# Kernel tuning notes

Measured on AMD Instinct MI355X. Metric: run time of the kernel, lower is better.

The kernel has to match this reference:

```python
import jax, jax.numpy as jnp
import numpy as np

# --- static config (lmax = mmax = 2, m-prime coefficient layout) ---
L = 2
NCOEF = (L + 1) ** 2            # 9 coeffs; m-prime order: m=0 -> l=0,1,2 | m=1 -> (-,+) x l=1,2 | m=2 -> (-,+) x l=2
GATE_IDX = jnp.array([0, 1, 0, 1, 0, 1, 1, 1])  # (l-1) of each non-scalar coeff in m-prime order
N_NODES = 10000
N_EDGES = 50000
C_SPH = 128
C_HID = 128
C_EDGE = 128
EXTRA_M0 = L * C_HID            # gate scalars emitted by conv1's m=0 branch


def _silu(x):
    return x * jax.nn.sigmoid(x)


def _layernorm(x, g, b, eps=1e-5):
    mu = jnp.mean(x, axis=-1, keepdims=True)
    var = jnp.var(x, axis=-1, keepdims=True)
    return (x - mu) * jax.lax.rsqrt(var + eps) * g + b


def _radial(x_edge, w1, b1, g, beta, w2, b2):
    # RadialFunction: Linear -> LayerNorm -> SiLU -> Linear, emits per-edge channel weights [E, 6*c_in]
    h = _silu(_layernorm(x_edge @ w1 + b1, g, beta))
    return h @ w2 + b2


def _so2_conv(feat, rad, w0, b0, w1, w2, c_in, c_out, extra):
    # feat: [E, 9, c_in] in m-prime order. Block-diagonal SO2 conv with per-edge radial modulation.
    E = feat.shape[0]
    # m = 0 block (3 real coeffs) -> dense linear, optionally emits extra gating scalars
    x0 = feat[:, 0:3].reshape(E, 3 * c_in) * rad[:, : 3 * c_in]
    y0 = x0 @ w0 + b0                                   # [E, 3*c_out + extra]
    out0 = y0[:, : 3 * c_out].reshape(E, 3, c_out)
    x_extra = y0[:, 3 * c_out:]
    # m = 1 block: coeffs 3:7 -> [E, 2(sign), 2(l)*c_in], complex-structured matmul
    x1 = feat[:, 3:7].reshape(E, 2, 2 * c_in) * rad[:, 3 * c_in: 5 * c_in][:, None, :]
    y1 = x1 @ w1                                        # [E, 2, 4*c_out]
    h = 2 * c_out
    r, i = y1[..., :h], y1[..., h:]
    out1 = jnp.stack([r[:, 0] - i[:, 1], r[:, 1] + i[:, 0]], axis=1).reshape(E, 4, c_out)
    # m = 2 block: coeffs 7:9 -> [E, 2(sign), 1(l)*c_in]
    x2 = feat[:, 7:9].reshape(E, 2, c_in) * rad[:, 5 * c_in: 6 * c_in][:, None, :]
    y2 = x2 @ w2                                        # [E, 2, 2*c_out]
    r, i = y2[..., :c_out], y2[..., c_out:]
    out2 = jnp.stack([r[:, 0] - i[:, 1], r[:, 1] + i[:, 0]], axis=1).reshape(E, 2, c_out)
    return jnp.concatenate([out0, out1, out2], axis=1), x_extra


def _gate(gating, feat):
    # GateActivation (m_prime=True): SiLU on l=0 scalar, SiLU(gates) broadcast per-degree on l>0 coeffs
    E = feat.shape[0]
    g = _silu(gating).reshape(E, L, C_HID)[:, GATE_IDX]  # [E, 8, C_HID]
    return jnp.concatenate([_silu(feat[:, :1]), feat[:, 1:] * g], axis=1)


def setup_inputs() -> dict:
    key = jax.random.key(0)
    ks = jax.random.split(key, 16)

    def nrm(k, shape, scale=1.0):
        return jax.random.normal(k, shape, dtype=jnp.float32) * scale

    C, H, CE = C_SPH, C_HID, C_EDGE
    return {
        "x": nrm(ks[0], (N_NODES, NCOEF, C)),
        "x_edge": nrm(ks[1], (N_EDGES, CE)),
        "edge_distance": jax.random.uniform(ks[2], (N_EDGES,), dtype=jnp.float32),
        "edge_index": jax.random.randint(ks[3], (2, N_EDGES), 0, N_NODES),
        "wigner": nrm(ks[4], (N_EDGES, NCOEF, NCOEF), 0.3),
        "wigner_inv": nrm(ks[5], (N_EDGES, NCOEF, NCOEF), 0.3),
        # radial MLP 1 (edge embed -> 6*C_SPH per-edge weights)
        "rad1_w1": nrm(ks[6], (CE, CE), CE ** -0.5),
        "rad1_b1": jnp.zeros((CE,), jnp.float32),
        "rad1_g": jnp.ones((CE,), jnp.float32),
        "rad1_beta": jnp.zeros((CE,), jnp.float32),
        "rad1_w2": nrm(ks[7], (CE, 6 * C), CE ** -0.5),
        "rad1_b2": jnp.zeros((6 * C,), jnp.float32),
        # SO2 conv 1 (sphere -> hidden, + gate scalars)
        "c1_w0": nrm(ks[8], (3 * C, 3 * H + EXTRA_M0), (3 * C) ** -0.5),
        "c1_b0": jnp.zeros((3 * H + EXTRA_M0,), jnp.float32),
        "c1_w1": nrm(ks[9], (2 * C, 4 * H), (2 * C) ** -0.5),
        "c1_w2": nrm(ks[10], (C, 2 * H), C ** -0.5),
        # radial MLP 2 (edge embed -> 6*C_HID per-edge weights)
        "rad2_w1": nrm(ks[11], (CE, CE), CE ** -0.5),
        "rad2_b1": jnp.zeros((CE,), jnp.float32),
        "rad2_g": jnp.ones((CE,), jnp.float32),
        "rad2_beta": jnp.zeros((CE,), jnp.float32),
        "rad2_w2": nrm(ks[12], (CE, 6 * H), CE ** -0.5),
        "rad2_b2": jnp.zeros((6 * H,), jnp.float32),
        # SO2 conv 2 (hidden -> sphere)
        "c2_w0": nrm(ks[13], (3 * H, 3 * C), (3 * H) ** -0.5),
        "c2_b0": jnp.zeros((3 * C,), jnp.float32),
        "c2_w1": nrm(ks[14], (2 * H, 4 * C), (2 * H) ** -0.5),
        "c2_w2": nrm(ks[15], (H, 2 * C), H ** -0.5),
    }


def reference(x, x_edge, edge_distance, edge_index, wigner, wigner_inv,
              rad1_w1, rad1_b1, rad1_g, rad1_beta, rad1_w2, rad1_b2,
              c1_w0, c1_b0, c1_w1, c1_w2,
              rad2_w1, rad2_b1, rad2_g, rad2_beta, rad2_w2, rad2_b2,
              c2_w0, c2_b0, c2_w1, c2_w2):
    src, dst = edge_index[0], edge_index[1]
    # gather source node features + per-edge Wigner rotation into m-prime layout: [E, 9, C_SPH]
    msg = jnp.einsum('erf,efc->erc', wigner, x[src])
    rad1 = _radial(x_edge, rad1_w1, rad1_b1, rad1_g, rad1_beta, rad1_w2, rad1_b2)
    msg, gating = _so2_conv(msg, rad1, c1_w0, c1_b0, c1_w1, c1_w2, C_SPH, C_HID, EXTRA_M0)
    msg = _gate(gating, msg)
    rad2 = _radial(x_edge, rad2_w1, rad2_b1, rad2_g, rad2_beta, rad2_w2, rad2_b2)
    msg, _ = _so2_conv(msg, rad2, c2_w0, c2_b0, c2_w1, c2_w2, C_HID, C_SPH, 0)
    # rotate back to the global frame and scatter-sum onto destination nodes
    msg = jnp.einsum('efr,erc->efc', wigner_inv, msg)
    return jax.ops.segment_sum(msg, dst, num_segments=x.shape[0])
```

## Files before the change

kernel.cpp:

```cpp
#include <hip/hip_runtime.h>
#include <hip/hip_bf16.h>

#define EDGES 50000
#define NODES 10000

typedef __hip_bfloat16 bf16;
typedef __attribute__((ext_vector_type(8))) short bf16x8v;
typedef __attribute__((ext_vector_type(4))) float f32x4;

__device__ __forceinline__ float bf2f(bf16 v){ return __bfloat162float(v); }
__device__ __forceinline__ bf16  f2bf(float v){ return __float2bfloat16(v); }
__device__ __forceinline__ unsigned short f2bfu(float f){
  bf16 h = __float2bfloat16(f);
  union{ bf16 h; unsigned short s; } u; u.h = h; return u.s;
}
__device__ __forceinline__ float silu_f(float v){ return v * (1.0f/(1.0f+__expf(-v))); }

__device__ __forceinline__ unsigned mul1(unsigned a, unsigned b){
  union{unsigned u; float f;} a0,a1,b0,b1;
  a0.u = (a & 0xffffu) << 16; a1.u = a & 0xffff0000u;
  b0.u = (b & 0xffffu) << 16; b1.u = b & 0xffff0000u;
  float p0 = a0.f*b0.f, p1 = a1.f*b1.f;
  return (unsigned)f2bfu(p0) | ((unsigned)f2bfu(p1) << 16);
}
__device__ __forceinline__ uint4 mulp(uint4 a, uint4 b){
  uint4 r; r.x=mul1(a.x,b.x); r.y=mul1(a.y,b.y); r.z=mul1(a.z,b.z); r.w=mul1(a.w,b.w); return r;
}

__global__ __launch_bounds__(256)
void k_wT(const float* __restrict__ w, bf16* __restrict__ wt, int K, int N){
  __shared__ float tile[32][33];
  const int kb = blockIdx.x*32, nb = blockIdx.y*32;
  const int tx = threadIdx.x & 31, ty = threadIdx.x >> 5;
#pragma unroll
  for (int i=0;i<32;i+=8) tile[ty+i][tx] = w[(size_t)(kb+ty+i)*N + nb+tx];
  __syncthreads();
#pragma unroll
  for (int i=0;i<32;i+=8) wt[(size_t)(nb+ty+i)*K + kb+tx] = f2bf(tile[tx][ty+i]);
}

__global__ __launch_bounds__(128)
void k_gather_rot(const float* __restrict__ x, const int* __restrict__ eidx,
                  const float* __restrict__ wig, bf16* __restrict__ msg)
{
  const int e = blockIdx.x;
  const int c = threadIdx.x;
  __shared__ float wl[81];
  if (c < 81) wl[c] = wig[e*81 + c];
  const int src = eidx[e];
  const float* xp = x + (size_t)src*1152 + c;
  float xr[9];
#pragma unroll
  for (int f=0; f<9; ++f) xr[f] = xp[f*128];
  __syncthreads();
  bf16* mp = msg + (size_t)e*1152 + c;
#pragma unroll
  for (int fo=0; fo<9; ++fo){
    float a = 0.f;
#pragma unroll
    for (int f=0; f<9; ++f) a = fmaf(wl[fo*9+f], xr[f], a);
    mp[fo*128] = f2bf(a);
  }
}

__global__ __launch_bounds__(256)
void k_radial(const float* __restrict__ x_edge,
              const float* __restrict__ w1, const float* __restrict__ b1,
              const float* __restrict__ gm, const float* __restrict__ bt,
              const float* __restrict__ w2, const float* __restrict__ b2,
              bf16* __restrict__ ro)
{
  __shared__ float xe[16][128];
  __shared__ float h[16][128];
  __shared__ float mu_s[16], rs_s[16];
  const int t = threadIdx.x;
  const int e0 = blockIdx.x * 16;
  for (int i=0;i<8;++i){
    int lin = t + 256*i;
    int e = lin >> 7, j2 = lin & 127;
    xe[e][j2] = x_edge[(size_t)(e0+e)*128 + j2];
  }
  __syncthreads();
  const int j = t & 127, g = t >> 7;
  {
    float acc[8] = {0,0,0,0,0,0,0,0};
    for (int k=0;k<128;k+=4){
      float wv0 = w1[(k+0)*128+j];
      float wv1 = w1[(k+1)*128+j];
      float wv2 = w1[(k+2)*128+j];
      float wv3 = w1[(k+3)*128+j];
#pragma unroll
      for (int e=0;e<8;++e){
        float4 xv = *(const float4*)&xe[g*8+e][k];
        acc[e] += xv.x*wv0 + xv.y*wv1 + xv.z*wv2 + xv.w*wv3;
      }
    }
    float bv = b1[j];
#pragma unroll
    for (int e=0;e<8;++e) h[g*8+e][j] = acc[e] + bv;
  }
  __syncthreads();
  {
    int e = t >> 4, p = t & 15;
    float s=0.f, ss=0.f;
#pragma unroll
    for (int i=0;i<8;++i){ float v = h[e][p+16*i]; s += v; ss += v*v; }
#pragma unroll
    for (int off=8; off>0; off>>=1){ s += __shfl_xor(s, off, 16); ss += __shfl_xor(ss, off, 16); }
    if (p==0){
      float m = s*(1.f/128.f);
      mu_s[e] = m;
      rs_s[e] = rsqrtf(fmaxf(ss*(1.f/128.f)-m*m, 0.f) + 1e-5f);
    }
  }
  __syncthreads();
  {
    float gv = gm[j], bv = bt[j];
#pragma unroll
    for (int e=0;e<8;++e){
      int ee = g*8+e;
      float v = (h[ee][j]-mu_s[ee])*rs_s[ee]*gv + bv;
      h[ee][j] = silu_f(v);
    }
  }
  __syncthreads();
  if (t < 192){
    int col = t*4;
    float acc[16][4];
#pragma unroll
    for (int e=0;e<16;++e){ acc[e][0]=acc[e][1]=acc[e][2]=acc[e][3]=0.f; }
    for (int k=0;k<128;k+=4){
      float4 wv0 = *(const float4*)&w2[(k+0)*768+col];
      float4 wv1 = *(const float4*)&w2[(k+1)*768+col];
      float4 wv2 = *(const float4*)&w2[(k+2)*768+col];
      float4 wv3 = *(const float4*)&w2[(k+3)*768+col];
#pragma unroll
      for (int e=0;e<16;++e){
        float4 hv = *(const float4*)&h[e][k];
        acc[e][0] += hv.x*wv0.x + hv.y*wv1.x + hv.z*wv2.x + hv.w*wv3.x;
        acc[e][1] += hv.x*wv0.y + hv.y*wv1.y + hv.z*wv2.y + hv.w*wv3.y;
        acc[e][2] += hv.x*wv0.z + hv.y*wv1.z + hv.z*wv2.z + hv.w*wv3.z;
        acc[e][3] += hv.x*wv0.w + hv.y*wv1.w + hv.z*wv2.w + hv.w*wv3.w;
      }
    }
    float4 bv = *(const float4*)&b2[col];
#pragma unroll
    for (int e=0;e<16;++e){
      ushort4 pk;
      pk.x = f2bfu(acc[e][0]+bv.x);
      pk.y = f2bfu(acc[e][1]+bv.y);
      pk.z = f2bfu(acc[e][2]+bv.z);
      pk.w = f2bfu(acc[e][3]+bv.w);
      *reinterpret_cast<ushort4*>(&ro[(size_t)(e0+e)*768 + col]) = pk;
    }
  }
}

template<bool CONV1>
__global__ __launch_bounds__(256, 3)
void k_so2_mfma(const bf16* __restrict__ rad,
                const bf16* __restrict__ w0t, const float* __restrict__ b0,
                const bf16* __restrict__ w1t, const bf16* __restrict__ w2t,
                bf16* __restrict__ msg)
{
  __shared__ char ldsA[32768];
  __shared__ bf16 gls[8192];
  const int t    = threadIdx.x;
  const int lane = t & 63, wv = t >> 6;
  const int lrow = lane & 15, lhi = lane >> 4;
  const int e0 = blockIdx.x * 32;
  int evalid = EDGES - e0; if (evalid > 32) evalid = 32;

#pragma unroll
  for (int i=0;i<6;++i){
    int ch = t + 256*i;
    int row = ch / 48, k0 = (ch % 48) * 8;
    int e = e0 + row;
    uint4 o = {0u,0u,0u,0u};
    if (e < EDGES){
      uint4 mz = *(const uint4*)(msg + (size_t)e*1152 + k0);
      uint4 rz = *(const uint4*)(rad + (size_t)e*768  + k0);
      o = mulp(mz, rz);
    }
    *(uint4*)(ldsA + ((row*768 + k0*2) ^ ((row&7)<<4))) = o;
  }
  __syncthreads();

  constexpr int NT0 = CONV1 ? 10 : 6;
  const int wcol0 = wv * NT0 * 16;
  f32x4 acc0[NT0][2];
  const f32x4 zf = {0.f,0.f,0.f,0.f};
#pragma unroll
  for (int nt=0; nt<NT0; ++nt){ acc0[nt][0]=zf; acc0[nt][1]=zf; }
  for (int ks=0; ks<12; ++ks){
    bf16x8v a0 = *(const bf16x8v*)(ldsA + (((lrow   )*768 + ks*64 + lhi*16) ^ ((lrow&7)<<4)));
    bf16x8v a1 = *(const bf16x8v*)(ldsA + (((16+lrow)*768 + ks*64 + lhi*16) ^ ((lrow&7)<<4)));
#pragma unroll
    for (int nt=0; nt<NT0; ++nt){
      int coln = wcol0 + nt*16 + lrow;
      bf16x8v b = *(const bf16x8v*)(w0t + (size_t)coln*384 + ks*32 + lhi*8);
      acc0[nt][0] = __builtin_amdgcn_mfma_f32_16x16x32_bf16(a0, b, acc0[nt][0], 0,0,0);
      acc0[nt][1] = __builtin_amdgcn_mfma_f32_16x16x32_bf16(a1, b, acc0[nt][1], 0,0,0);
    }
  }
  if (CONV1){
#pragma unroll
    for (int nt=0; nt<NT0; ++nt){
      int colb = wcol0 + nt*16;
      if (colb >= 384){
        float bc = b0[colb + lrow];
#pragma unroll
        for (int mt=0; mt<2; ++mt)
#pragma unroll
        for (int r=0; r<4; ++r){
          int el = mt*16 + lhi*4 + r;
          gls[el*256 + colb + lrow - 384] = f2bf(silu_f(acc0[nt][mt][r] + bc));
        }
      }
    }
  }
  __syncthreads();
#pragma unroll
  for (int nt=0; nt<NT0; ++nt){
    int colb = wcol0 + nt*16;
    if (colb < 384){
      int col = colb + lrow;
      int f = col >> 7, c = col & 127;
      float bc = b0[col];
#pragma unroll
      for (int mt=0; mt<2; ++mt)
#pragma unroll
      for (int r=0; r<4; ++r){
        int el = mt*16 + lhi*4 + r;
        if (el < evalid){
          float v = acc0[nt][mt][r] + bc;
          float o;
          if (CONV1) o = (f==0) ? silu_f(v) : v * bf2f(gls[el*256 + (f==2?128:0) + c]);
          else       o = v;
          msg[(size_t)(e0+el)*1152 + col] = f2bf(o);
        }
      }
    }
  }

#pragma unroll
  for (int i=0;i<8;++i){
    int ch = t + 256*i;
    int row = ch >> 5, k0 = (ch & 31) * 8;
    int e = e0 + (row >> 1);
    uint4 o = {0u,0u,0u,0u};
    if (e < EDGES){
      uint4 mz = *(const uint4*)(msg + (size_t)e*1152 + 384 + (row&1)*256 + k0);
      uint4 rz = *(const uint4*)(rad + (size_t)e*768  + 384 + k0);
      o = mulp(mz, rz);
    }
    *(uint4*)(ldsA + ((row*512 + k0*2) ^ ((row&7)<<4))) = o;
  }
  __syncthreads();

#pragma unroll
  for (int half=0; half<2; ++half){
    f32x4 acc1[4][2][2];
#pragma unroll
    for (int p=0;p<4;++p){ acc1[p][0][0]=zf; acc1[p][0][1]=zf; acc1[p][1][0]=zf; acc1[p][1][1]=zf; }
    for (int ks=0; ks<8; ++ks){
      bf16x8v aA[2];
#pragma unroll
      for (int m2=0; m2<2; ++m2){
        int row = (half*2+m2)*16 + lrow;
        aA[m2] = *(const bf16x8v*)(ldsA + ((row*512 + ks*64 + lhi*16) ^ ((row&7)<<4)));
      }
#pragma unroll
      for (int p=0; p<4; ++p){
        int jj = wv*64 + p*16 + lrow;
        bf16x8v br = *(const bf16x8v*)(w1t + (size_t)jj*256       + ks*32 + lhi*8);
        bf16x8v bi = *(const bf16x8v*)(w1t + (size_t)(jj+256)*256 + ks*32 + lhi*8);
#pragma unroll
        for (int m2=0;m2<2;++m2){
          acc1[p][m2][0] = __builtin_amdgcn_mfma_f32_16x16x32_bf16(aA[m2], br, acc1[p][m2][0], 0,0,0);
          acc1[p][m2][1] = __builtin_amdgcn_mfma_f32_16x16x32_bf16(aA[m2], bi, acc1[p][m2][1], 0,0,0);
        }
      }
    }
#pragma unroll
    for (int p=0;p<4;++p)
#pragma unroll
    for (int m2=0;m2<2;++m2){
      int mt = half*2 + m2;
#pragma unroll
      for (int re=0;re<2;++re){
        int el = mt*8 + lhi*2 + re;
        float r0 = acc1[p][m2][0][2*re+0], r1 = acc1[p][m2][0][2*re+1];
        float i0 = acc1[p][m2][1][2*re+0], i1 = acc1[p][m2][1][2*re+1];
        float o0 = r0 - i1, o1 = r1 + i0;
        int jj = wv*64 + p*16 + lrow;
        if (CONV1){ float g = bf2f(gls[el*256 + jj]); o0 *= g; o1 *= g; }
        if (el < evalid){
          size_t base = (size_t)(e0+el)*1152;
          msg[base + 384 + jj] = f2bf(o0);
          msg[base + 640 + jj] = f2bf(o1);
        }
      }
    }
  }
  __syncthreads();

#pragma unroll
  for (int i=0;i<4;++i){
    int ch = t + 256*i;
    int row = ch >> 4, k0 = (ch & 15) * 8;
    int e = e0 + (row >> 1);
    uint4 o = {0u,0u,0u,0u};
    if (e < EDGES){
      uint4 mz = *(const uint4*)(msg + (size_t)e*1152 + 896 + (row&1)*128 + k0);
      uint4 rz = *(const uint4*)(rad + (size_t)e*768  + 640 + k0);
      o = mulp(mz, rz);
    }
    *(uint4*)(ldsA + ((row*256 + k0*2) ^ ((row&7)<<4))) = o;
  }
  __syncthreads();

  {
    f32x4 acc2[2][4][2];
#pragma unroll
    for (int p=0;p<2;++p)
#pragma unroll
    for (int mt=0;mt<4;++mt){ acc2[p][mt][0]=zf; acc2[p][mt][1]=zf; }
    for (int ks=0; ks<4; ++ks){
      bf16x8v aA[4];
#pragma unroll
      for (int mt=0;mt<4;++mt){
        int row = mt*16 + lrow;
        aA[mt] = *(const bf16x8v*)(ldsA + ((row*256 + ks*64 + lhi*16) ^ ((row&7)<<4)));
      }
#pragma unroll
      for (int p=0;p<2;++p){
        int jj = wv*32 + p*16 + lrow;
        bf16x8v br = *(const bf16x8v*)(w2t + (size_t)jj*128       + ks*32 + lhi*8);
        bf16x8v bi = *(const bf16x8v*)(w2t + (size_t)(jj+128)*128 + ks*32 + lhi*8);
#pragma unroll
        for (int mt=0;mt<4;++mt){
          acc2[p][mt][0] = __builtin_amdgcn_mfma_f32_16x16x32_bf16(aA[mt], br, acc2[p][mt][0], 0,0,0);
          acc2[p][mt][1] = __builtin_amdgcn_mfma_f32_16x16x32_bf16(aA[mt], bi, acc2[p][mt][1], 0,0,0);
        }
      }
    }
#pragma unroll
    for (int p=0;p<2;++p)
#pragma unroll
    for (int mt=0;mt<4;++mt)
#pragma unroll
    for (int re=0;re<2;++re){
      int el = mt*8 + lhi*2 + re;
      float r0 = acc2[p][mt][0][2*re+0], r1 = acc2[p][mt][0][2*re+1];
      float i0 = acc2[p][mt][1][2*re+0], i1 = acc2[p][mt][1][2*re+1];
      float o0 = r0 - i1, o1 = r1 + i0;
      int jj = wv*32 + p*16 + lrow;
      if (CONV1){ float g = bf2f(gls[el*256 + 128 + jj]); o0 *= g; o1 *= g; }
      if (el < evalid){
        size_t base = (size_t)(e0+el)*1152;
        msg[base + 896  + jj] = f2bf(o0);
        msg[base + 1024 + jj] = f2bf(o1);
      }
    }
  }
}

__global__ __launch_bounds__(128)
void k_wiginv_scatter(const bf16* __restrict__ msg, const int* __restrict__ eidx,
                      const float* __restrict__ wiginv, float* __restrict__ out)
{
  const int e = blockIdx.x;
  const int c = threadIdx.x;
  __shared__ float wl[81];
  if (c < 81) wl[c] = wiginv[e*81 + c];
  float m[9];
#pragma unroll
  for (int r=0;r<9;++r) m[r] = bf2f(msg[(size_t)e*1152 + r*128 + c]);
  const int dst = eidx[EDGES + e];
  __syncthreads();
  float* op = out + (size_t)dst*1152 + c;
#pragma unroll
  for (int f=0;f<9;++f){
    float a = 0.f;
#pragma unroll
    for (int r=0;r<9;++r) a = fmaf(wl[f*9+r], m[r], a);
    atomicAdd(op + f*128, a);
  }
}

extern "C" void kernel_launch(void* const* d_in, const int* in_sizes, int n_in,
                              void* d_out, int out_size, void* d_ws, size_t ws_size,
                              hipStream_t stream)
{
  const float* x       = (const float*)d_in[0];
  const float* x_edge  = (const float*)d_in[1];
  const int*   eidx    = (const int*)  d_in[3];
  const float* wig     = (const float*)d_in[4];
  const float* wiginv  = (const float*)d_in[5];
  const float* r1w1    = (const float*)d_in[6];
  const float* r1b1    = (const float*)d_in[7];
  const float* r1g     = (const float*)d_in[8];
  const float* r1bt    = (const float*)d_in[9];
  const float* r1w2    = (const float*)d_in[10];
  const float* r1b2    = (const float*)d_in[11];
  const float* c1w0    = (const float*)d_in[12];
  const float* c1b0    = (const float*)d_in[13];
  const float* c1w1    = (const float*)d_in[14];
  const float* c1w2    = (const float*)d_in[15];
  const float* r2w1    = (const float*)d_in[16];
  const float* r2b1    = (const float*)d_in[17];
  const float* r2g     = (const float*)d_in[18];
  const float* r2bt    = (const float*)d_in[19];
  const float* r2w2    = (const float*)d_in[20];
  const float* r2b2    = (const float*)d_in[21];
  const float* c2w0    = (const float*)d_in[22];
  const float* c2b0    = (const float*)d_in[23];
  const float* c2w1    = (const float*)d_in[24];
  const float* c2w2    = (const float*)d_in[25];
  float* out = (float*)d_out;

  char* ws = (char*)d_ws;
  bf16* msg  = (bf16*)(ws);
  bf16* rad  = (bf16*)(ws + (size_t)115200000);
  bf16* w0t1 = (bf16*)(ws + (size_t)192000000);
  bf16* w1t1 = (bf16*)(ws + (size_t)192491520);
  bf16* w2t1 = (bf16*)(ws + (size_t)192753664);
  bf16* w0t2 = (bf16*)(ws + (size_t)192819200);
  bf16* w1t2 = (bf16*)(ws + (size_t)193114112);
  bf16* w2t2 = (bf16*)(ws + (size_t)193376256);

  k_wT<<<dim3(12,20),256,0,stream>>>(c1w0, w0t1, 384, 640);
  k_wT<<<dim3( 8,16),256,0,stream>>>(c1w1, w1t1, 256, 512);
  k_wT<<<dim3( 4, 8),256,0,stream>>>(c1w2, w2t1, 128, 256);
  k_wT<<<dim3(12,12),256,0,stream>>>(c2w0, w0t2, 384, 384);
  k_wT<<<dim3( 8,16),256,0,stream>>>(c2w1, w1t2, 256, 512);
  k_wT<<<dim3( 4, 8),256,0,stream>>>(c2w2, w2t2, 128, 256);

  hipMemsetAsync(d_out, 0, (size_t)out_size*sizeof(float), stream);
  k_gather_rot<<<EDGES, 128, 0, stream>>>(x, eidx, wig, msg);
  k_radial<<<EDGES/16, 256, 0, stream>>>(x_edge, r1w1, r1b1, r1g, r1bt, r1w2, r1b2, rad);
  k_so2_mfma<true ><<<(EDGES+31)/32, 256, 0, stream>>>(rad, w0t1, c1b0, w1t1, w2t1, msg);
  k_radial<<<EDGES/16, 256, 0, stream>>>(x_edge, r2w1, r2b1, r2g, r2bt, r2w2, r2b2, rad);
  k_so2_mfma<false><<<(EDGES+31)/32, 256, 0, stream>>>(rad, w0t2, c2b0, w1t2, w2t2, msg);
  k_wiginv_scatter<<<EDGES, 128, 0, stream>>>(msg, eidx, wiginv, out);
}
```

Baseline: 1.471 ms.

## Split fused SO2 conv kernel into per-m-block kernels with global gate buffer

The single fused SO2 conv kernel is split into three kernels, one per m-block (m=0, m=1, m=2), with the gate scalars written to a global buffer instead of shared memory. The m=1 kernel uses 16-edge blocks to create more blocks, and weight loads are batched ahead of the MFMA sequences to hide latency. The aim is smaller LDS per kernel, better occupancy and shorter dependency chains, at the cost of extra launches and re-reading msg, rad and gate data from global memory.

```diff
diff --git a/kernel.cpp b/kernel.cpp
--- a/kernel.cpp
+++ b/kernel.cpp
@@ -156,51 +156,60 @@
   }
 }
 
+
 template<bool CONV1>
 __global__ __launch_bounds__(256, 3)
-void k_so2_mfma(const bf16* __restrict__ rad,
-                const bf16* __restrict__ w0t, const float* __restrict__ b0,
-                const bf16* __restrict__ w1t, const bf16* __restrict__ w2t,
-                bf16* __restrict__ msg)
-{
-  __shared__ char ldsA[32768];
+void k_g0(const bf16* __restrict__ rad, const bf16* __restrict__ msg_in,
+          const bf16* __restrict__ w0t, const float* __restrict__ b0,
+          bf16* __restrict__ msg, bf16* __restrict__ glb)
+{
+  __shared__ char ldsA[24576];
   __shared__ bf16 gls[8192];
-  const int t    = threadIdx.x;
+  const int t = threadIdx.x;
   const int lane = t & 63, wv = t >> 6;
   const int lrow = lane & 15, lhi = lane >> 4;
   const int e0 = blockIdx.x * 32;
   int evalid = EDGES - e0; if (evalid > 32) evalid = 32;
+  const uint4 z4 = {0u,0u,0u,0u};
+  const f32x4 zf = {0.f,0.f,0.f,0.f};
 
 #pragma unroll
   for (int i=0;i<6;++i){
     int ch = t + 256*i;
     int row = ch / 48, k0 = (ch % 48) * 8;
     int e = e0 + row;
-    uint4 o = {0u,0u,0u,0u};
+    uint4 mz = z4, rz = z4;
     if (e < EDGES){
-      uint4 mz = *(const uint4*)(msg + (size_t)e*1152 + k0);
-      uint4 rz = *(const uint4*)(rad + (size_t)e*768  + k0);
-      o = mulp(mz, rz);
-    }
-    *(uint4*)(ldsA + ((row*768 + k0*2) ^ ((row&7)<<4))) = o;
+      mz = *(const uint4*)(msg_in + (size_t)e*1152 + k0);
+      rz = *(const uint4*)(rad    + (size_t)e*768  + k0);
+    }
+    *(uint4*)(ldsA + ((row*768 + k0*2) ^ ((row&7)<<4))) = mulp(mz, rz);
   }
   __syncthreads();
 
   constexpr int NT0 = CONV1 ? 10 : 6;
+  constexpr int HB  = NT0 / 2;
   const int wcol0 = wv * NT0 * 16;
   f32x4 acc0[NT0][2];
-  const f32x4 zf = {0.f,0.f,0.f,0.f};
 #pragma unroll
   for (int nt=0; nt<NT0; ++nt){ acc0[nt][0]=zf; acc0[nt][1]=zf; }
   for (int ks=0; ks<12; ++ks){
     bf16x8v a0 = *(const bf16x8v*)(ldsA + (((lrow   )*768 + ks*64 + lhi*16) ^ ((lrow&7)<<4)));
     bf16x8v a1 = *(const bf16x8v*)(ldsA + (((16+lrow)*768 + ks*64 + lhi*16) ^ ((lrow&7)<<4)));
 #pragma unroll
-    for (int nt=0; nt<NT0; ++nt){
-      int coln = wcol0 + nt*16 + lrow;
-      bf16x8v b = *(const bf16x8v*)(w0t + (size_t)coln*384 + ks*32 + lhi*8);
-      acc0[nt][0] = __builtin_amdgcn_mfma_f32_16x16x32_bf16(a0, b, acc0[nt][0], 0,0,0);
-      acc0[nt][1] = __builtin_amdgcn_mfma_f32_16x16x32_bf16(a1, b, acc0[nt][1], 0,0,0);
+    for (int h=0; h<2; ++h){
+      bf16x8v bb[HB];
+#pragma unroll
+      for (int j=0;j<HB;++j){
+        int coln = wcol0 + (h*HB+j)*16 + lrow;
+        bb[j] = *(const bf16x8v*)(w0t + (size_t)coln*384 + ks*32 + lhi*8);
+      }
+#pragma unroll
+      for (int j=0;j<HB;++j){
+        int nt = h*HB+j;
+        acc0[nt][0] = __builtin_amdgcn_mfma_f32_16x16x32_bf16(a0, bb[j], acc0[nt][0], 0,0,0);
+        acc0[nt][1] = __builtin_amdgcn_mfma_f32_16x16x32_bf16(a1, bb[j], acc0[nt][1], 0,0,0);
+      }
     }
   }
   if (CONV1){
@@ -209,17 +218,20 @@
       int colb = wcol0 + nt*16;
       if (colb >= 384){
         float bc = b0[colb + lrow];
+        int cc = colb + lrow - 384;
 #pragma unroll
         for (int mt=0; mt<2; ++mt)
 #pragma unroll
         for (int r=0; r<4; ++r){
           int el = mt*16 + lhi*4 + r;
-          gls[el*256 + colb + lrow - 384] = f2bf(silu_f(acc0[nt][mt][r] + bc));
+          bf16 gv = f2bf(silu_f(acc0[nt][mt][r] + bc));
+          gls[el*256 + cc] = gv;
+          if (el < evalid) glb[(size_t)(e0+el)*256 + cc] = gv;
         }
       }
     }
-  }
-  __syncthreads();
+    __syncthreads();
+  }
 #pragma unroll
   for (int nt=0; nt<NT0; ++nt){
     int colb = wcol0 + nt*16;
@@ -242,126 +254,154 @@
       }
     }
   }
-
-#pragma unroll
-  for (int i=0;i<8;++i){
+}
+
+template<bool CONV1>
+__global__ __launch_bounds__(256, 3)
+void k_g1(const bf16* __restrict__ rad,
+          const bf16* __restrict__ w1t,
+          bf16* __restrict__ msg, const bf16* __restrict__ glb)
+{
+  __shared__ char ldsA[16384];
+  const int t = threadIdx.x;
+  const int lane = t & 63, wv = t >> 6;
+  const int lrow = lane & 15, lhi = lane >> 4;
+  const int e0 = blockIdx.x * 16;
+  const uint4 z4 = {0u,0u,0u,0u};
+  const f32x4 zf = {0.f,0.f,0.f,0.f};
+
+#pragma unroll
+  for (int i=0;i<4;++i){
     int ch = t + 256*i;
     int row = ch >> 5, k0 = (ch & 31) * 8;
     int e = e0 + (row >> 1);
-    uint4 o = {0u,0u,0u,0u};
+    uint4 mz = z4, rz = z4;
     if (e < EDGES){
-      uint4 mz = *(const uint4*)(msg + (size_t)e*1152 + 384 + (row&1)*256 + k0);
-      uint4 rz = *(const uint4*)(rad + (size_t)e*768  + 384 + k0);
-      o = mulp(mz, rz);
-    }
-    *(uint4*)(ldsA + ((row*512 + k0*2) ^ ((row&7)<<4))) = o;
-  }
-  __syncthreads();
-
-#pragma unroll
-  for (int half=0; half<2; ++half){
-    f32x4 acc1[4][2][2];
-#pragma unroll
-    for (int p=0;p<4;++p){ acc1[p][0][0]=zf; acc1[p][0][1]=zf; acc1[p][1][0]=zf; acc1[p][1][1]=zf; }
-    for (int ks=0; ks<8; ++ks){
-      bf16x8v aA[2];
-#pragma unroll
-      for (int m2=0; m2<2; ++m2){
-        int row = (half*2+m2)*16 + lrow;
-        aA[m2] = *(const bf16x8v*)(ldsA + ((row*512 + ks*64 + lhi*16) ^ ((row&7)<<4)));
-      }
-#pragma unroll
-      for (int p=0; p<4; ++p){
-        int jj = wv*64 + p*16 + lrow;
-        bf16x8v br = *(const bf16x8v*)(w1t + (size_t)jj*256       + ks*32 + lhi*8);
-        bf16x8v bi = *(const bf16x8v*)(w1t + (size_t)(jj+256)*256 + ks*32 + lhi*8);
-#pragma unroll
-        for (int m2=0;m2<2;++m2){
-          acc1[p][m2][0] = __builtin_amdgcn_mfma_f32_16x16x32_bf16(aA[m2], br, acc1[p][m2][0], 0,0,0);
-          acc1[p][m2][1] = __builtin_amdgcn_mfma_f32_16x16x32_bf16(aA[m2], bi, acc1[p][m2][1], 0,0,0);
-        }
-      }
-    }
-#pragma unroll
-    for (int p=0;p<4;++p)
+      mz = *(const uint4*)(msg + (size_t)e*1152 + 384 + (row&1)*256 + k0);
+      rz = *(const uint4*)(rad + (size_t)e*768  + 384 + k0);
+    }
+    *(uint4*)(ldsA + ((row*512 + k0*2) ^ ((row&7)<<4))) = mulp(mz, rz);
+  }
+  __syncthreads();
+
+  f32x4 acc1[4][2][2];
+#pragma unroll
+  for (int p=0;p<4;++p){ acc1[p][0][0]=zf; acc1[p][0][1]=zf; acc1[p][1][0]=zf; acc1[p][1][1]=zf; }
+  for (int ks=0; ks<8; ++ks){
+    bf16x8v aA[2];
+#pragma unroll
+    for (int m2=0; m2<2; ++m2){
+      int row = m2*16 + lrow;
+      aA[m2] = *(const bf16x8v*)(ldsA + ((row*512 + ks*64 + lhi*16) ^ ((row&7)<<4)));
+    }
+    bf16x8v br[4], bi[4];
+#pragma unroll
+    for (int p=0; p<4; ++p){
+      int jj = wv*64 + p*16 + lrow;
+      br[p] = *(const bf16x8v*)(w1t + (size_t)jj*256       + ks*32 + lhi*8);
+      bi[p] = *(const bf16x8v*)(w1t + (size_t)(jj+256)*256 + ks*32 + lhi*8);
+    }
+#pragma unroll
+    for (int p=0; p<4; ++p)
 #pragma unroll
     for (int m2=0;m2<2;++m2){
-      int mt = half*2 + m2;
-#pragma unroll
-      for (int re=0;re<2;++re){
-        int el = mt*8 + lhi*2 + re;
-        float r0 = acc1[p][m2][0][2*re+0], r1 = acc1[p][m2][0][2*re+1];
-        float i0 = acc1[p][m2][1][2*re+0], i1 = acc1[p][m2][1][2*re+1];
-        float o0 = r0 - i1, o1 = r1 + i0;
-        int jj = wv*64 + p*16 + lrow;
-        if (CONV1){ float g = bf2f(gls[el*256 + jj]); o0 *= g; o1 *= g; }
-        if (el < evalid){
-          size_t base = (size_t)(e0+el)*1152;
-          msg[base + 384 + jj] = f2bf(o0);
-          msg[base + 640 + jj] = f2bf(o1);
-        }
-      }
-    }
-  }
-  __syncthreads();
+      acc1[p][m2][0] = __builtin_amdgcn_mfma_f32_16x16x32_bf16(aA[m2], br[p], acc1[p][m2][0], 0,0,0);
+      acc1[p][m2][1] = __builtin_amdgcn_mfma_f32_16x16x32_bf16(aA[m2], bi[p], acc1[p][m2][1], 0,0,0);
+    }
+  }
+#pragma unroll
+  for (int p=0;p<4;++p)
+#pragma unroll
+  for (int m2=0;m2<2;++m2)
+#pragma unroll
+  for (int re=0;re<2;++re){
+    int elL = m2*8 + lhi*2 + re;
+    int e = e0 + elL;
+    if (e < EDGES){
+      float r0 = acc1[p][m2][0][2*re+0], r1 = acc1[p][m2][0][2*re+1];
+      float i0 = acc1[p][m2][1][2*re+0], i1 = acc1[p][m2][1][2*re+1];
+      float o0 = r0 - i1, o1 = r1 + i0;
+      int jj = wv*64 + p*16 + lrow;
+      if (CONV1){ float g = bf2f(glb[(size_t)e*256 + jj]); o0 *= g; o1 *= g; }
+      size_t base = (size_t)e*1152;
+      msg[base + 384 + jj] = f2bf(o0);
+      msg[base + 640 + jj] = f2bf(o1);
+    }
+  }
+}
+
+template<bool CONV1>
+__global__ __launch_bounds__(256, 3)
+void k_g2(const bf16* __restrict__ rad,
+          const bf16* __restrict__ w2t,
+          bf16* __restrict__ msg, const bf16* __restrict__ glb)
+{
+  __shared__ char ldsA[16384];
+  const int t = threadIdx.x;
+  const int lane = t & 63, wv = t >> 6;
+  const int lrow = lane & 15, lhi = lane >> 4;
+  const int e0 = blockIdx.x * 32;
+  const uint4 z4 = {0u,0u,0u,0u};
+  const f32x4 zf = {0.f,0.f,0.f,0.f};
 
 #pragma unroll
   for (int i=0;i<4;++i){
     int ch = t + 256*i;
     int row = ch >> 4, k0 = (ch & 15) * 8;
     int e = e0 + (row >> 1);
-    uint4 o = {0u,0u,0u,0u};
+    uint4 mz = z4, rz = z4;
     if (e < EDGES){
-      uint4 mz = *(const uint4*)(msg + (size_t)e*1152 + 896 + (row&1)*128 + k0);
-      uint4 rz = *(const uint4*)(rad + (size_t)e*768  + 640 + k0);
-      o = mulp(mz, rz);
-    }
-    *(uint4*)(ldsA + ((row*256 + k0*2) ^ ((row&7)<<4))) = o;
-  }
-  __syncthreads();
-
-  {
-    f32x4 acc2[2][4][2];
+      mz = *(const uint4*)(msg + (size_t)e*1152 + 896 + (row&1)*128 + k0);
+      rz = *(const uint4*)(rad + (size_t)e*768  + 640 + k0);
+    }
+    *(uint4*)(ldsA + ((row*256 + k0*2) ^ ((row&7)<<4))) = mulp(mz, rz);
+  }
+  __syncthreads();
+
+  f32x4 acc2[2][4][2];
+#pragma unroll
+  for (int p=0;p<2;++p)
+#pragma unroll
+  for (int mt=0;mt<4;++mt){ acc2[p][mt][0]=zf; acc2[p][mt][1]=zf; }
+  for (int ks=0; ks<4; ++ks){
+    bf16x8v aA[4];
+#pragma unroll
+    for (int mt=0;mt<4;++mt){
+      int row = mt*16 + lrow;
+      aA[mt] = *(const bf16x8v*)(ldsA + ((row*256 + ks*64 + lhi*16) ^ ((row&7)<<4)));
+    }
+    bf16x8v br2[2], bi2[2];
+#pragma unroll
+    for (int p=0;p<2;++p){
+      int jj = wv*32 + p*16 + lrow;
+      br2[p] = *(const bf16x8v*)(w2t + (size_t)jj*128       + ks*32 + lhi*8);
+      bi2[p] = *(const bf16x8v*)(w2t + (size_t)(jj+128)*128 + ks*32 + lhi*8);
+    }
 #pragma unroll
     for (int p=0;p<2;++p)
 #pragma unroll
-    for (int mt=0;mt<4;++mt){ acc2[p][mt][0]=zf; acc2[p][mt][1]=zf; }
-    for (int ks=0; ks<4; ++ks){
-      bf16x8v aA[4];
-#pragma unroll
-      for (int mt=0;mt<4;++mt){
-        int row = mt*16 + lrow;
-        aA[mt] = *(const bf16x8v*)(ldsA + ((row*256 + ks*64 + lhi*16) ^ ((row&7)<<4)));
-      }
-#pragma unroll
-      for (int p=0;p<2;++p){
-        int jj = wv*32 + p*16 + lrow;
-        bf16x8v br = *(const bf16x8v*)(w2t + (size_t)jj*128       + ks*32 + lhi*8);
-        bf16x8v bi = *(const bf16x8v*)(w2t + (size_t)(jj+128)*128 + ks*32 + lhi*8);
-#pragma unroll
-        for (int mt=0;mt<4;++mt){
-          acc2[p][mt][0] = __builtin_amdgcn_mfma_f32_16x16x32_bf16(aA[mt], br, acc2[p][mt][0], 0,0,0);
-          acc2[p][mt][1] = __builtin_amdgcn_mfma_f32_16x16x32_bf16(aA[mt], bi, acc2[p][mt][1], 0,0,0);
-        }
-      }
-    }
-#pragma unroll
-    for (int p=0;p<2;++p)
-#pragma unroll
-    for (int mt=0;mt<4;++mt)
-#pragma unroll
-    for (int re=0;re<2;++re){
-      int el = mt*8 + lhi*2 + re;
+    for (int mt=0;mt<4;++mt){
+      acc2[p][mt][0] = __builtin_amdgcn_mfma_f32_16x16x32_bf16(aA[mt], br2[p], acc2[p][mt][0], 0,0,0);
+      acc2[p][mt][1] = __builtin_amdgcn_mfma_f32_16x16x32_bf16(aA[mt], bi2[p], acc2[p][mt][1], 0,0,0);
+    }
+  }
+#pragma unroll
+  for (int p=0;p<2;++p)
+#pragma unroll
+  for (int mt=0;mt<4;++mt)
+#pragma unroll
+  for (int re=0;re<2;++re){
+    int el = mt*8 + lhi*2 + re;
+    int e = e0 + el;
+    if (e < EDGES){
       float r0 = acc2[p][mt][0][2*re+0], r1 = acc2[p][mt][0][2*re+1];
       float i0 = acc2[p][mt][1][2*re+0], i1 = acc2[p][mt][1][2*re+1];
       float o0 = r0 - i1, o1 = r1 + i0;
       int jj = wv*32 + p*16 + lrow;
-      if (CONV1){ float g = bf2f(gls[el*256 + 128 + jj]); o0 *= g; o1 *= g; }
-      if (el < evalid){
-        size_t base = (size_t)(e0+el)*1152;
-        msg[base + 896  + jj] = f2bf(o0);
-        msg[base + 1024 + jj] = f2bf(o1);
-      }
+      if (CONV1){ float g = bf2f(glb[(size_t)e*256 + 128 + jj]); o0 *= g; o1 *= g; }
+      size_t base = (size_t)e*1152;
+      msg[base + 896  + jj] = f2bf(o0);
+      msg[base + 1024 + jj] = f2bf(o1);
     }
   }
 }
@@ -429,6 +469,7 @@
   bf16* w0t2 = (bf16*)(ws + (size_t)192819200);
   bf16* w1t2 = (bf16*)(ws + (size_t)193114112);
   bf16* w2t2 = (bf16*)(ws + (size_t)193376256);
+  bf16* glb  = (bf16*)(ws + (size_t)193441792);
 
   k_wT<<<dim3(12,20),256,0,stream>>>(c1w0, w0t1, 384, 640);
   k_wT<<<dim3( 8,16),256,0,stream>>>(c1w1, w1t1, 256, 512);
@@ -439,9 +480,16 @@
 
   hipMemsetAsync(d_out, 0, (size_t)out_size*sizeof(float), stream);
   k_gather_rot<<<EDGES, 128, 0, stream>>>(x, eidx, wig, msg);
+
   k_radial<<<EDGES/16, 256, 0, stream>>>(x_edge, r1w1, r1b1, r1g, r1bt, r1w2, r1b2, rad);
-  k_so2_mfma<true ><<<(EDGES+31)/32, 256, 0, stream>>>(rad, w0t1, c1b0, w1t1, w2t1, msg);
+  k_g0<true ><<<(EDGES+31)/32, 256, 0, stream>>>(rad, msg, w0t1, c1b0, msg, glb);
+  k_g1<true ><<<(EDGES+15)/16, 256, 0, stream>>>(rad, w1t1, msg, glb);
+  k_g2<true ><<<(EDGES+31)/32, 256, 0, stream>>>(rad, w2t1, msg, glb);
+
   k_radial<<<EDGES/16, 256, 0, stream>>>(x_edge, r2w1, r2b1, r2g, r2bt, r2w2, r2b2, rad);
-  k_so2_mfma<false><<<(EDGES+31)/32, 256, 0, stream>>>(rad, w0t2, c2b0, w1t2, w2t2, msg);
+  k_g0<false><<<(EDGES+31)/32, 256, 0, stream>>>(rad, msg, w0t2, c2b0, msg, glb);
+  k_g1<false><<<(EDGES+15)/16, 256, 0, stream>>>(rad, w1t2, msg, glb);
+  k_g2<false><<<(EDGES+31)/32, 256, 0, stream>>>(rad, w2t2, msg, glb);
+
   k_wiginv_scatter<<<EDGES, 128, 0, stream>>>(msg, eidx, wiginv, out);
 }
```

After: 1.416 ms. 1.04x faster.
